# Performance work log

Measured on AMD Instinct MI355X. Metric: run time of the kernel, lower is better.

## Reference

```python
import jax, jax.numpy as jnp
import numpy as np

B, S, ENC, DEC, ATTN = 32, 4096, 512, 512, 512


def setup_inputs() -> dict:
    key = jax.random.key(0)
    k1, k2, k3, k4, k5, k6 = jax.random.split(key, 6)
    h = jax.random.normal(k1, (B, DEC), dtype=jnp.float32)
    enc_out = jax.random.normal(k2, (B, S, ENC), dtype=jnp.float32)
    mask = jax.random.randint(k3, (B, S), 0, 2).astype(bool)
    # torch nn.Linear(in, out, bias=False): y = x @ W.T with W [out, in].
    # Store weights as [in, out] so y = x @ W; same math.
    sc = 1.0 / np.sqrt(DEC)
    W_h = jax.random.normal(k4, (DEC, ATTN), dtype=jnp.float32) * sc
    W_s = jax.random.normal(k5, (ENC, ATTN), dtype=jnp.float32) * sc
    v = jax.random.normal(k6, (ATTN,), dtype=jnp.float32) * sc
    return {"h": h, "enc_out": enc_out, "mask": mask, "W_h": W_h, "W_s": W_s, "v": v}


def reference(h, enc_out, mask, W_h, W_s, v):
    # query: [B, 1, A]; key: [B, S, A]
    query = (h @ W_h)[:, None, :]
    key = jnp.einsum("bse,ea->bsa", enc_out, W_s)
    energy = jnp.tanh(query + key)                    # [B, S, A]
    score = jnp.einsum("bsa,a->bs", energy, v)        # v^T tanh(...)
    score = jnp.where(mask, jnp.float32(-1e9), score)
    attn = jax.nn.softmax(score, axis=-1)             # [B, S]
    ctx = jnp.einsum("bs,bse->be", attn, enc_out)     # weighted sum
    return (ctx, attn)
```

## Files before the change

### kernel.cpp

```cpp
#include <hip/hip_runtime.h>
#include <hip/hip_bf16.h>
#include <math.h>

#define BB 32
#define SS 4096
#define EE 512
#define AA 512

typedef short bf16x8 __attribute__((ext_vector_type(8)));
typedef float f32x4 __attribute__((ext_vector_type(4)));
typedef unsigned short u16x4 __attribute__((ext_vector_type(4)));

__device__ __forceinline__ unsigned short f2bf(float f) {
  unsigned int u = __float_as_uint(f);
  u += 0x7fffu + ((u >> 16) & 1u);
  return (unsigned short)(u >> 16);
}

__device__ __forceinline__ float bf2f(unsigned short s) {
  return __uint_as_float(((unsigned int)s) << 16);
}

__device__ __forceinline__ float tanh_fast(float x) {
  return 1.f - 2.f / (__expf(2.f * x) + 1.f);
}

__global__ void query_kernel(const float* __restrict__ h,
                             const float* __restrict__ Wh,
                             float* __restrict__ q) {
  __shared__ float hrow[EE];
  int b = blockIdx.x;
  int t = threadIdx.x;
  for (int i = t; i < EE; i += 256) hrow[i] = h[b * EE + i];
  __syncthreads();
  float a0 = 0.f, a1 = 0.f;
  for (int e = 0; e < EE; ++e) {
    float hv = hrow[e];
    a0 += hv * Wh[e * AA + t];
    a1 += hv * Wh[e * AA + t + 256];
  }
  q[b * AA + t] = a0;
  q[b * AA + t + 256] = a1;
}

__global__ void wst_kernel(const float* __restrict__ Ws,
                           unsigned short* __restrict__ Wst) {
  int i = blockIdx.x * 256 + threadIdx.x;
  int a = i >> 9, e = i & 511;
  Wst[a * EE + e] = f2bf(Ws[e * AA + a]);
}

__global__ __launch_bounds__(256, 2) void fused_kernel(
    const float* __restrict__ enc, const unsigned short* __restrict__ Wst,
    const float* __restrict__ q, const float* __restrict__ v,
    const int* __restrict__ mask,
    float* __restrict__ rawscore,
    float* __restrict__ ctxp,
    float* __restrict__ mbuf) {
  __shared__ __align__(16) unsigned short Atile[64 * 512];
  __shared__ float spart[4][64];
  __shared__ float wrow[64];
  __shared__ float pbuf[4][512];
  const int b = blockIdx.y, chunk = blockIdx.x;
  const int s0 = chunk * 64;
  const int tid = threadIdx.x;

  const float4* src = (const float4*)(enc + ((size_t)b * SS + s0) * EE);
  for (int pass = 0; pass < 2; ++pass) {
#pragma unroll
    for (int i = 0; i < 16; ++i) {
      int idx = (pass * 16 + i) * 256 + tid;
      float4 x = src[idx];
      int row = idx >> 7;
      int c4 = idx & 127;
      int ch = c4 >> 1;
      int within = (c4 & 1) * 4;
      int cs = ch ^ (row & 7);
      u16x4 p;
      p.x = f2bf(x.x); p.y = f2bf(x.y); p.z = f2bf(x.z); p.w = f2bf(x.w);
      *(u16x4*)&Atile[row * 512 + cs * 8 + within] = p;
    }
  }
  __syncthreads();

  const int w = tid >> 6, lane = tid & 63;
  const int quad = lane >> 4, l16 = lane & 15;

  float srow[4][4];
#pragma unroll
  for (int m = 0; m < 4; ++m)
#pragma unroll
    for (int r = 0; r < 4; ++r) srow[m][r] = 0.f;

  for (int h = 0; h < 2; ++h) {
    const int n0 = w * 128 + h * 64;
    f32x4 acc[4][4];
#pragma unroll
    for (int m = 0; m < 4; ++m)
#pragma unroll
      for (int n = 0; n < 4; ++n) acc[m][n] = (f32x4){0.f, 0.f, 0.f, 0.f};

    const unsigned short* wb = Wst + (size_t)(n0 + l16) * EE + quad * 8;
#pragma unroll 2
    for (int k0 = 0; k0 < 512; k0 += 32) {
      int cs = ((k0 >> 3) + quad) ^ (l16 & 7);
      bf16x8 aF[4], bF[4];
#pragma unroll
      for (int m = 0; m < 4; ++m)
        aF[m] = *(const bf16x8*)&Atile[(m * 16 + l16) * 512 + cs * 8];
#pragma unroll
      for (int n = 0; n < 4; ++n)
        bF[n] = *(const bf16x8*)&wb[(size_t)n * 16 * EE + k0];
#pragma unroll
      for (int m = 0; m < 4; ++m)
#pragma unroll
        for (int n = 0; n < 4; ++n)
          acc[m][n] =
              __builtin_amdgcn_mfma_f32_16x16x32_bf16(aF[m], bF[n], acc[m][n], 0, 0, 0);
    }
#pragma unroll
    for (int n = 0; n < 4; ++n) {
      float qn = q[b * AA + n0 + n * 16 + l16];
      float vn = v[n0 + n * 16 + l16];
#pragma unroll
      for (int m = 0; m < 4; ++m)
#pragma unroll
        for (int r = 0; r < 4; ++r)
          srow[m][r] += tanh_fast(qn + acc[m][n][r]) * vn;
    }
  }

#pragma unroll
  for (int m = 0; m < 4; ++m)
#pragma unroll
    for (int r = 0; r < 4; ++r) {
      float s = srow[m][r];
      s += __shfl_xor(s, 1, 64);
      s += __shfl_xor(s, 2, 64);
      s += __shfl_xor(s, 4, 64);
      s += __shfl_xor(s, 8, 64);
      if (l16 == 0) spart[w][m * 16 + quad * 4 + r] = s;
    }
  __syncthreads();

  if (tid < 64) {
    float raw = spart[0][tid] + spart[1][tid] + spart[2][tid] + spart[3][tid];
    float sc = mask[(size_t)b * SS + s0 + tid] ? -1e9f : raw;
    rawscore[(size_t)b * SS + s0 + tid] = sc;
    float mx = sc;
    for (int off = 1; off < 64; off <<= 1)
      mx = fmaxf(mx, __shfl_xor(mx, off, 64));
    wrow[tid] = __expf(sc - mx);
    if (tid == 0) mbuf[b * 64 + chunk] = mx;
  }
  __syncthreads();

  {
    const int c = tid & 63;
    const int sg = tid >> 6;
    float a8[8] = {0.f, 0.f, 0.f, 0.f, 0.f, 0.f, 0.f, 0.f};
#pragma unroll
    for (int i = 0; i < 16; ++i) {
      int row = sg * 16 + i;
      float wgt = wrow[row];
      bf16x8 av = *(const bf16x8*)&Atile[row * 512 + ((c ^ (row & 7)) * 8)];
#pragma unroll
      for (int j = 0; j < 8; ++j)
        a8[j] += wgt * bf2f((unsigned short)av[j]);
    }
#pragma unroll
    for (int j = 0; j < 8; ++j) pbuf[sg][c * 8 + j] = a8[j];
  }
  __syncthreads();
#pragma unroll
  for (int jj = 0; jj < 2; ++jj) {
    int e = jj * 256 + tid;
    ctxp[((size_t)b * 64 + chunk) * EE + e] =
        pbuf[0][e] + pbuf[1][e] + pbuf[2][e] + pbuf[3][e];
  }
}

__global__ void finalize_kernel(float* __restrict__ attn,
                                const float* __restrict__ ctxp,
                                const float* __restrict__ mbuf,
                                float* __restrict__ ctx) {
  __shared__ float red[8];
  __shared__ float fc[64];
  int b = blockIdx.x, t = threadIdx.x;
  float* row = attn + (size_t)b * SS;
  float vals[16];
  float m = -3e38f;
#pragma unroll
  for (int i = 0; i < 16; ++i) {
    float x = row[i * 256 + t];
    vals[i] = x;
    m = fmaxf(m, x);
  }
  for (int off = 1; off < 64; off <<= 1) m = fmaxf(m, __shfl_xor(m, off, 64));
  int wv = t >> 6, ln = t & 63;
  if (ln == 0) red[wv] = m;
  __syncthreads();
  m = fmaxf(fmaxf(red[0], red[1]), fmaxf(red[2], red[3]));
  float sum = 0.f;
#pragma unroll
  for (int i = 0; i < 16; ++i) { vals[i] = __expf(vals[i] - m); sum += vals[i]; }
  for (int off = 1; off < 64; off <<= 1) sum += __shfl_xor(sum, off, 64);
  if (ln == 0) red[4 + wv] = sum;
  __syncthreads();
  sum = red[4] + red[5] + red[6] + red[7];
  float inv = 1.f / sum;
#pragma unroll
  for (int i = 0; i < 16; ++i) row[i * 256 + t] = vals[i] * inv;

  if (t < 64) fc[t] = __expf(mbuf[b * 64 + t] - m) * inv;
  __syncthreads();
#pragma unroll
  for (int jj = 0; jj < 2; ++jj) {
    int e = jj * 256 + t;
    const float* p = ctxp + (size_t)b * 64 * EE + e;
    float s = 0.f;
#pragma unroll
    for (int c = 0; c < 64; ++c) s += fc[c] * p[c * EE];
    ctx[b * EE + e] = s;
  }
}

extern "C" void kernel_launch(void* const* d_in, const int* in_sizes, int n_in,
                              void* d_out, int out_size, void* d_ws, size_t ws_size,
                              hipStream_t stream) {
  const float* h    = (const float*)d_in[0];
  const float* enc  = (const float*)d_in[1];
  const int*   mask = (const int*)d_in[2];
  const float* Wh   = (const float*)d_in[3];
  const float* Ws   = (const float*)d_in[4];
  const float* v    = (const float*)d_in[5];

  float* out  = (float*)d_out;
  float* ctx  = out;
  float* attn = out + BB * EE;

  char* ws = (char*)d_ws;
  float* qws = (float*)ws;                         ws += (size_t)BB * AA * 4;
  unsigned short* Wst = (unsigned short*)ws;       ws += (size_t)AA * EE * 2;
  float* ctxp = (float*)ws;                        ws += (size_t)BB * 64 * EE * 4;
  float* mbuf = (float*)ws;

  hipLaunchKernelGGL(query_kernel, dim3(32), dim3(256), 0, stream, h, Wh, qws);
  hipLaunchKernelGGL(wst_kernel, dim3(1024), dim3(256), 0, stream, Ws, Wst);
  hipLaunchKernelGGL(fused_kernel, dim3(SS / 64, BB), dim3(256), 0, stream,
                     enc, Wst, qws, v, mask, attn, ctxp, mbuf);
  hipLaunchKernelGGL(finalize_kernel, dim3(BB), dim3(256), 0, stream,
                     attn, ctxp, mbuf, ctx);
}
```

Measured before the change: 538.3 us.

## Drop LDS staging of encoder tile; feed MFMA directly from global memory

The fused kernel no longer converts the 64x512 encoder tile into a swizzled bf16 LDS buffer. Each wave loads fp32 rows from global memory and packs them to bf16 fragments just before the MFMA. The context partial sum also re-reads fp32 encoder rows from global instead of LDS. With the LDS and the extra barrier gone, occupancy is raised to 3 blocks per CU, but the same encoder data is now fetched repeatedly by each wave and pass, relying on caches.

Result: slower. 735.3 us (+36.6%).

```diff
diff --git a/kernel.cpp b/kernel.cpp
--- a/kernel.cpp
+++ b/kernel.cpp
@@ -9,7 +9,6 @@
 
 typedef short bf16x8 __attribute__((ext_vector_type(8)));
 typedef float f32x4 __attribute__((ext_vector_type(4)));
-typedef unsigned short u16x4 __attribute__((ext_vector_type(4)));
 
 __device__ __forceinline__ unsigned short f2bf(float f) {
   unsigned int u = __float_as_uint(f);
@@ -17,12 +16,17 @@
   return (unsigned short)(u >> 16);
 }
 
-__device__ __forceinline__ float bf2f(unsigned short s) {
-  return __uint_as_float(((unsigned int)s) << 16);
-}
-
 __device__ __forceinline__ float tanh_fast(float x) {
   return 1.f - 2.f / (__expf(2.f * x) + 1.f);
+}
+
+__device__ __forceinline__ bf16x8 pack8(float4 a, float4 b) {
+  union { bf16x8 v; __hip_bfloat162 h[4]; } u;
+  u.h[0] = __float22bfloat162_rn(make_float2(a.x, a.y));
+  u.h[1] = __float22bfloat162_rn(make_float2(a.z, a.w));
+  u.h[2] = __float22bfloat162_rn(make_float2(b.x, b.y));
+  u.h[3] = __float22bfloat162_rn(make_float2(b.z, b.w));
+  return u.v;
 }
 
 __global__ void query_kernel(const float* __restrict__ h,
@@ -50,41 +54,26 @@
   Wst[a * EE + e] = f2bf(Ws[e * AA + a]);
 }
 
-__global__ __launch_bounds__(256, 2) void fused_kernel(
+__global__ __launch_bounds__(256, 3) void fused_kernel(
     const float* __restrict__ enc, const unsigned short* __restrict__ Wst,
     const float* __restrict__ q, const float* __restrict__ v,
     const int* __restrict__ mask,
     float* __restrict__ rawscore,
     float* __restrict__ ctxp,
     float* __restrict__ mbuf) {
-  __shared__ __align__(16) unsigned short Atile[64 * 512];
   __shared__ float spart[4][64];
   __shared__ float wrow[64];
-  __shared__ float pbuf[4][512];
   const int b = blockIdx.y, chunk = blockIdx.x;
   const int s0 = chunk * 64;
   const int tid = threadIdx.x;
-
-  const float4* src = (const float4*)(enc + ((size_t)b * SS + s0) * EE);
-  for (int pass = 0; pass < 2; ++pass) {
-#pragma unroll
-    for (int i = 0; i < 16; ++i) {
-      int idx = (pass * 16 + i) * 256 + tid;
-      float4 x = src[idx];
-      int row = idx >> 7;
-      int c4 = idx & 127;
-      int ch = c4 >> 1;
-      int within = (c4 & 1) * 4;
-      int cs = ch ^ (row & 7);
-      u16x4 p;
-      p.x = f2bf(x.x); p.y = f2bf(x.y); p.z = f2bf(x.z); p.w = f2bf(x.w);
-      *(u16x4*)&Atile[row * 512 + cs * 8 + within] = p;
-    }
-  }
-  __syncthreads();
-
   const int w = tid >> 6, lane = tid & 63;
   const int quad = lane >> 4, l16 = lane & 15;
+
+  const float* encB = enc + (size_t)b * SS * EE;
+  const float* aPtr[4];
+#pragma unroll
+  for (int m = 0; m < 4; ++m)
+    aPtr[m] = encB + (size_t)(s0 + m * 16 + l16) * EE + quad * 8;
 
   float srow[4][4];
 #pragma unroll
@@ -101,13 +90,15 @@
       for (int n = 0; n < 4; ++n) acc[m][n] = (f32x4){0.f, 0.f, 0.f, 0.f};
 
     const unsigned short* wb = Wst + (size_t)(n0 + l16) * EE + quad * 8;
-#pragma unroll 2
+#pragma unroll 4
     for (int k0 = 0; k0 < 512; k0 += 32) {
-      int cs = ((k0 >> 3) + quad) ^ (l16 & 7);
       bf16x8 aF[4], bF[4];
 #pragma unroll
-      for (int m = 0; m < 4; ++m)
-        aF[m] = *(const bf16x8*)&Atile[(m * 16 + l16) * 512 + cs * 8];
+      for (int m = 0; m < 4; ++m) {
+        float4 f0 = *(const float4*)(aPtr[m] + k0);
+        float4 f1 = *(const float4*)(aPtr[m] + k0 + 4);
+        aF[m] = pack8(f0, f1);
+      }
 #pragma unroll
       for (int n = 0; n < 4; ++n)
         bF[n] = *(const bf16x8*)&wb[(size_t)n * 16 * EE + k0];
@@ -115,8 +106,8 @@
       for (int m = 0; m < 4; ++m)
 #pragma unroll
         for (int n = 0; n < 4; ++n)
-          acc[m][n] =
-              __builtin_amdgcn_mfma_f32_16x16x32_bf16(aF[m], bF[n], acc[m][n], 0, 0, 0);
+          acc[m][n] = __builtin_amdgcn_mfma_f32_16x16x32_bf16(
+              aF[m], bF[n], acc[m][n], 0, 0, 0);
     }
 #pragma unroll
     for (int n = 0; n < 4; ++n) {
@@ -156,27 +147,18 @@
   __syncthreads();
 
   {
-    const int c = tid & 63;
-    const int sg = tid >> 6;
-    float a8[8] = {0.f, 0.f, 0.f, 0.f, 0.f, 0.f, 0.f, 0.f};
-#pragma unroll
-    for (int i = 0; i < 16; ++i) {
-      int row = sg * 16 + i;
+    const int e0 = tid * 2;
+    float ax = 0.f, ay = 0.f;
+    const float* ep = encB + (size_t)s0 * EE + e0;
+#pragma unroll 8
+    for (int row = 0; row < 64; ++row) {
       float wgt = wrow[row];
-      bf16x8 av = *(const bf16x8*)&Atile[row * 512 + ((c ^ (row & 7)) * 8)];
-#pragma unroll
-      for (int j = 0; j < 8; ++j)
-        a8[j] += wgt * bf2f((unsigned short)av[j]);
-    }
-#pragma unroll
-    for (int j = 0; j < 8; ++j) pbuf[sg][c * 8 + j] = a8[j];
-  }
-  __syncthreads();
-#pragma unroll
-  for (int jj = 0; jj < 2; ++jj) {
-    int e = jj * 256 + tid;
-    ctxp[((size_t)b * 64 + chunk) * EE + e] =
-        pbuf[0][e] + pbuf[1][e] + pbuf[2][e] + pbuf[3][e];
+      float2 ev = *(const float2*)(ep + (size_t)row * EE);
+      ax += wgt * ev.x;
+      ay += wgt * ev.y;
+    }
+    float2 o = make_float2(ax, ay);
+    *(float2*)&ctxp[((size_t)b * 64 + chunk) * EE + e0] = o;
   }
 }
 
@@ -240,9 +222,9 @@
   float* attn = out + BB * EE;
 
   char* ws = (char*)d_ws;
-  float* qws = (float*)ws;                         ws += (size_t)BB * AA * 4;
-  unsigned short* Wst = (unsigned short*)ws;       ws += (size_t)AA * EE * 2;
-  float* ctxp = (float*)ws;                        ws += (size_t)BB * 64 * EE * 4;
+  float* qws = (float*)ws;                    ws += (size_t)BB * AA * 4;
+  unsigned short* Wst = (unsigned short*)ws;  ws += (size_t)AA * EE * 2;
+  float* ctxp = (float*)ws;                   ws += (size_t)BB * 64 * EE * 4;
   float* mbuf = (float*)ws;
 
   hipLaunchKernelGGL(query_kernel, dim3(32), dim3(256), 0, stream, h, Wh, qws);
```
